# Optimization experiments

Measured on AMD Instinct MI355X. Metric: run time of the kernel, lower is better.

## Reference

```python
import jax, jax.numpy as jnp
import numpy as np

NUM_HEADS = 8
HEAD_DIM = 64  # embed_dim 512 / 8 heads


def setup_inputs() -> dict:
    key = jax.random.key(0)
    k1, k2, k3 = jax.random.split(key, 3)
    B, S, D = 2, 4096, 512
    # xavier-uniform-ish scales for faithfulness to init (values don't affect math)
    x = jax.random.normal(k1, (B, S, D), dtype=jnp.float32)
    qkv_w = jax.random.normal(k2, (3 * D, D), dtype=jnp.float32) * (1.0 / np.sqrt(D))
    qkv_b = jnp.zeros((3 * D,), dtype=jnp.float32)
    o_w = jax.random.normal(k3, (D, D), dtype=jnp.float32) * (1.0 / np.sqrt(D))
    o_b = jnp.zeros((D,), dtype=jnp.float32)
    return {"x": x, "qkv_w": qkv_w, "qkv_b": qkv_b, "o_w": o_w, "o_b": o_b}


def reference(x, qkv_w, qkv_b, o_w, o_b):
    B, S, D = x.shape
    H, hd = NUM_HEADS, HEAD_DIM
    # qkv projection: torch Linear is x @ W^T + b
    qkv = jnp.einsum('bsd,ed->bse', x, qkv_w) + qkv_b        # [B, S, 3D]
    qkv = qkv.reshape(B, S, H, 3 * hd).transpose(0, 2, 1, 3)  # [B, H, S, 3hd]
    q, k, v = jnp.split(qkv, 3, axis=-1)                      # each [B, H, S, hd]
    scale = 1.0 / jnp.sqrt(jnp.float32(hd))
    logits = jnp.einsum('bhqd,bhkd->bhqk', q, k) * scale      # [B, H, S, S]
    attn = jax.nn.softmax(logits, axis=-1)
    vals = jnp.einsum('bhqk,bhkd->bhqd', attn, v)             # [B, H, S, hd]
    vals = vals.transpose(0, 2, 1, 3).reshape(B, S, D)        # [B, S, D]
    o = jnp.einsum('bsd,ed->bse', vals, o_w) + o_b            # [B, S, D]
    return o
```

## Files before the change

kernel.cpp:

```cpp
#include <hip/hip_runtime.h>
#include <hip/hip_bf16.h>


typedef __attribute__((ext_vector_type(8)))  __bf16 bf16x8;
typedef __attribute__((ext_vector_type(2)))  __bf16 bf16x2;
typedef __attribute__((ext_vector_type(4))) float  f32x4;
typedef __attribute__((ext_vector_type(16))) float  f32x16;

__device__ __forceinline__ unsigned cvtpk(float a, float b) {
    bf16x2 t; t.x = (__bf16)a; t.y = (__bf16)b;
    union { bf16x2 v; unsigned u; } u; u.v = t; return u.u;
}
#if __has_builtin(__builtin_amdgcn_exp2f)
__device__ __forceinline__ float fexp2(float x) { return __builtin_amdgcn_exp2f(x); }
#else
__device__ __forceinline__ float fexp2(float x) { return exp2f(x); }
#endif
__device__ __forceinline__ void gload16(const unsigned short* g, unsigned short* l) {
    __builtin_amdgcn_global_load_lds(
        (const __attribute__((address_space(1))) void*)g,
        (__attribute__((address_space(3))) void*)l, 16, 0, 0);
}

__device__ __forceinline__ int swz(int row, int col) {
    return row * 64 + (col ^ ((row & 7) << 3));
}

__global__ __launch_bounds__(256) void qkv_qk_gemm(
    const float* __restrict__ X, const float* __restrict__ W,
    const float* __restrict__ bias,
    unsigned short* __restrict__ Qb, unsigned short* __restrict__ Kb)
{
    __shared__ __attribute__((aligned(16))) unsigned short SH[128 * 144];
    unsigned short* As = &SH[0];
    unsigned short* Bs = &SH[8192];
    const int tid = threadIdx.x;
    const int wid = tid >> 6, lane = tid & 63;
    const int hi = lane >> 4, lo = lane & 15;
    const int wm = wid >> 1, wn = wid & 1;
    const int m0 = blockIdx.x * 128;
    const int by3 = blockIdx.y & 3, tt = blockIdx.y >> 2;
    const float QSCL = 0.125f * 1.44269504088896f;
    const float sc = (tt == 0) ? QSCL : 1.0f;

    f32x4 acc[4][4] = {};

    for (int k0 = 0; k0 < 512; k0 += 64) {
        __syncthreads();
        #pragma unroll
        for (int i = 0; i < 8; ++i) {
            const int c = i * 256 + tid;
            const int row = c >> 4, kc = (c & 15) << 2;
            const float4 va = *(const float4*)(X + (size_t)(m0 + row) * 512 + k0 + kc);
            uint2 pa; pa.x = cvtpk(va.x, va.y); pa.y = cvtpk(va.z, va.w);
            *(uint2*)&As[swz(row, kc)] = pa;
            const int nW = (by3 * 2 + (row >> 6)) * 192 + tt * 64 + (row & 63);
            const float4 vb = *(const float4*)(W + (size_t)nW * 512 + k0 + kc);
            uint2 pb; pb.x = cvtpk(vb.x, vb.y); pb.y = cvtpk(vb.z, vb.w);
            *(uint2*)&Bs[swz(row, kc)] = pb;
        }
        __syncthreads();
        #pragma unroll
        for (int ks = 0; ks < 2; ++ks) {
            bf16x8 af[4], bfr[4];
            #pragma unroll
            for (int mi = 0; mi < 4; ++mi)
                af[mi] = *(const bf16x8*)&As[swz(wm * 64 + mi * 16 + lo, ks * 32 + hi * 8)];
            #pragma unroll
            for (int ni = 0; ni < 4; ++ni)
                bfr[ni] = *(const bf16x8*)&Bs[swz(wn * 64 + ni * 16 + lo, ks * 32 + hi * 8)];
            #pragma unroll
            for (int mi = 0; mi < 4; ++mi)
                #pragma unroll
                for (int ni = 0; ni < 4; ++ni)
                    acc[mi][ni] = __builtin_amdgcn_mfma_f32_16x16x32_bf16(
                        bfr[ni], af[mi], acc[mi][ni], 0, 0, 0);
        }
    }
    __syncthreads();

    {
        const int hq = by3 * 2 + wn;
        #pragma unroll
        for (int ni = 0; ni < 4; ++ni) {
            const float4 bv4 = *(const float4*)&bias[hq * 192 + tt * 64 + ni * 16 + hi * 4];
            #pragma unroll
            for (int mi = 0; mi < 4; ++mi) {
                const int srow_ = wm * 64 + mi * 16 + lo;
                uint2 w;
                w.x = cvtpk((acc[mi][ni][0] + bv4.x) * sc, (acc[mi][ni][1] + bv4.y) * sc);
                w.y = cvtpk((acc[mi][ni][2] + bv4.z) * sc, (acc[mi][ni][3] + bv4.w) * sc);
                *(uint2*)&SH[srow_ * 144 + wn * 72 + ni * 16 + hi * 4] = w;
            }
        }
    }
    __syncthreads();

    const int b = m0 >> 12, sb = m0 & 4095;
    unsigned short* dst = tt ? Kb : Qb;
    #pragma unroll
    for (int c = 0; c < 2; ++c) {
        const int h = by3 * 2 + c;
        #pragma unroll
        for (int qq = 0; qq < 4; ++qq) {
            const int slot = qq * 256 + tid;
            const int row = slot >> 3, g = slot & 7;
            const uint4 v = *(const uint4*)&SH[row * 144 + c * 72 + g * 8];
            *(uint4*)(dst + (((size_t)(b * 8 + h)) * 4096 + sb + row) * 64 + g * 8) = v;
        }
    }
}

__global__ __launch_bounds__(256) void qkv_v_gemm(
    const float* __restrict__ X, const float* __restrict__ W,
    const float* __restrict__ bias, unsigned short* __restrict__ Vtg)
{
    __shared__ __attribute__((aligned(16))) unsigned short SH[128 * 144];
    unsigned short* As = &SH[0];
    unsigned short* Bs = &SH[8192];
    const int tid = threadIdx.x;
    const int wid = tid >> 6, lane = tid & 63;
    const int hi = lane >> 4, lo = lane & 15;
    const int wm = wid >> 1, wn = wid & 1;
    const int m0 = blockIdx.x * 128;
    const int by = blockIdx.y;

    f32x4 acc[4][4] = {};

    for (int k0 = 0; k0 < 512; k0 += 64) {
        __syncthreads();
        #pragma unroll
        for (int i = 0; i < 8; ++i) {
            const int c = i * 256 + tid;
            const int row = c >> 4, kc = (c & 15) << 2;
            const float4 va = *(const float4*)(X + (size_t)(m0 + row) * 512 + k0 + kc);
            uint2 pa; pa.x = cvtpk(va.x, va.y); pa.y = cvtpk(va.z, va.w);
            *(uint2*)&As[swz(row, kc)] = pa;
            const int nW = (by * 2 + (row >> 6)) * 192 + 128 + (row & 63);
            const float4 vb = *(const float4*)(W + (size_t)nW * 512 + k0 + kc);
            uint2 pb; pb.x = cvtpk(vb.x, vb.y); pb.y = cvtpk(vb.z, vb.w);
            *(uint2*)&Bs[swz(row, kc)] = pb;
        }
        __syncthreads();
        #pragma unroll
        for (int ks = 0; ks < 2; ++ks) {
            bf16x8 af[4], bfr[4];
            #pragma unroll
            for (int mi = 0; mi < 4; ++mi)
                af[mi] = *(const bf16x8*)&As[swz(wm * 64 + mi * 16 + lo, ks * 32 + hi * 8)];
            #pragma unroll
            for (int ni = 0; ni < 4; ++ni)
                bfr[ni] = *(const bf16x8*)&Bs[swz(wn * 64 + ni * 16 + lo, ks * 32 + hi * 8)];
            #pragma unroll
            for (int mi = 0; mi < 4; ++mi)
                #pragma unroll
                for (int ni = 0; ni < 4; ++ni)
                    acc[mi][ni] = __builtin_amdgcn_mfma_f32_16x16x32_bf16(
                        af[mi], bfr[ni], acc[mi][ni], 0, 0, 0);
        }
    }
    __syncthreads();

    #pragma unroll
    for (int ni = 0; ni < 4; ++ni) {
        const int d = ni * 16 + lo;
        const float bv = bias[(by * 2 + wn) * 192 + 128 + d];
        #pragma unroll
        for (int mi = 0; mi < 4; ++mi) {
            const int ml = wm * 64 + mi * 16 + hi * 4;
            uint2 w;
            w.x = cvtpk(acc[mi][ni][0] + bv, acc[mi][ni][1] + bv);
            w.y = cvtpk(acc[mi][ni][2] + bv, acc[mi][ni][3] + bv);
            *(uint2*)&SH[wn * 8704 + d * 136 + ml] = w;
        }
    }
    __syncthreads();

    const int b = m0 >> 12, sb = m0 & 4095;
    #pragma unroll
    for (int qq = 0; qq < 8; ++qq) {
        const int slot = qq * 256 + tid;
        const int c = slot >> 10, d = (slot >> 4) & 63, gc = slot & 15;
        const int h = by * 2 + c;
        const uint4 v = *(const uint4*)&SH[c * 8704 + d * 136 + gc * 8];
        *(uint4*)(Vtg + ((size_t)((b * 8 + h) * 64 + d)) * 4096 + sb + gc * 8) = v;
    }
}

__global__ __launch_bounds__(512, 2) void attn_fwd(
    const unsigned short* __restrict__ Qb,
    const unsigned short* __restrict__ Kb,
    const unsigned short* __restrict__ Vtg,
    unsigned short* __restrict__ Ob)
{
    __shared__ __attribute__((aligned(16))) unsigned short smem[6][4096];

    const int tid = threadIdx.x;
    const int wid = tid >> 6, lane = tid & 63;
    const int l31 = lane & 31, hl = lane >> 5;
    const int n_ = blockIdx.x;
    const int bh = (n_ & 7) * 2 + ((n_ >> 3) & 1);
    const int qb = n_ >> 4;
    const int b = bh >> 3, h = bh & 7;
    const int q0 = qb * 256 + wid * 32;
    const size_t kbase = (size_t)bh * 4096 * 64;
    const size_t vbase = (size_t)bh * 64 * 4096;

    const int srow = tid >> 3;
    const int sg = (tid & 7) ^ (srow & 7);
    const unsigned short* kS = Kb + kbase + (size_t)srow * 64 + sg * 8;
    const unsigned short* vS = Vtg + vbase + (size_t)srow * 4096 + sg * 8;

    bf16x8 qf[4];
    #pragma unroll
    for (int dk = 0; dk < 4; ++dk)
        qf[dk] = *(const bf16x8*)(Qb + kbase + (size_t)(q0 + l31) * 64 + dk * 16 + hl * 8);

    f32x16 o0 = {}, o1 = {};
    float l_run = 0.0f;

    const int s7 = l31 & 7;
    const int baseA = l31 * 64, baseB = (32 + l31) * 64;
    const int hl4 = hl * 4;

    gload16(kS, &smem[0][tid * 8]);
    gload16(vS, &smem[3][tid * 8]);
    gload16(kS + 4096, &smem[1][tid * 8]);
    gload16(vS + 64, &smem[4][tid * 8]);
    asm volatile("s_waitcnt vmcnt(2)" ::: "memory");
    __builtin_amdgcn_s_barrier();
    __builtin_amdgcn_sched_barrier(0);

    for (int t = 0; t < 64; ++t) {
        const int cur = t % 3;
        if (t < 62) {
            const int nb = (t + 2) % 3;
            gload16(kS + (size_t)(t + 2) * 4096, &smem[nb][tid * 8]);
            gload16(vS + (size_t)(t + 2) * 64, &smem[3 + nb][tid * 8]);
        }
        const unsigned short* KT = &smem[cur][0];
        const unsigned short* VT = &smem[3 + cur][0];

        f32x16 s0 = {}, s1 = {};
        __builtin_amdgcn_s_setprio(1);
        #pragma unroll
        for (int dk = 0; dk < 4; ++dk) {
            const int g = dk * 2 + hl;
            const bf16x8 kA = *(const bf16x8*)(KT + baseA + 8 * (g ^ s7));
            const bf16x8 kB = *(const bf16x8*)(KT + baseB + 8 * (g ^ s7));
            s0 = __builtin_amdgcn_mfma_f32_32x32x16_bf16(kA, qf[dk], s0, 0, 0, 0);
            s1 = __builtin_amdgcn_mfma_f32_32x32x16_bf16(kB, qf[dk], s1, 0, 0, 0);
        }
        __builtin_amdgcn_s_setprio(0);

        #pragma unroll
        for (int i = 0; i < 16; ++i) {
            s0[i] = fexp2(s0[i]);
            s1[i] = fexp2(s1[i]);
        }
        float lsA = 0.f, lsB = 0.f, lsC = 0.f, lsD = 0.f;
        #pragma unroll
        for (int i = 0; i < 4; ++i) {
            lsA += s0[i];      lsB += s0[i + 4];
            lsA += s0[i + 8];  lsB += s0[i + 12];
            lsC += s1[i];      lsD += s1[i + 4];
            lsC += s1[i + 8];  lsD += s1[i + 12];
        }
        l_run += (lsA + lsB) + (lsC + lsD);

        union U8 { unsigned u[4]; bf16x8 v; };
        U8 p0, p1, p2, p3;
        #pragma unroll
        for (int i = 0; i < 4; ++i) {
            p0.u[i] = cvtpk(s0[2 * i],     s0[2 * i + 1]);
            p1.u[i] = cvtpk(s0[2 * i + 8], s0[2 * i + 9]);
            p2.u[i] = cvtpk(s1[2 * i],     s1[2 * i + 1]);
            p3.u[i] = cvtpk(s1[2 * i + 8], s1[2 * i + 9]);
        }
        const bf16x8 pf[4] = { p0.v, p1.v, p2.v, p3.v };

        __builtin_amdgcn_s_setprio(1);
        #pragma unroll
        for (int ks = 0; ks < 4; ++ks) {
            const int gA = ((2 * ks) ^ s7) << 3, gB = ((2 * ks + 1) ^ s7) << 3;
            union { uint2 u2[2]; bf16x8 v; } va, vb;
            va.u2[0] = *(const uint2*)(VT + baseA + gA + hl4);
            va.u2[1] = *(const uint2*)(VT + baseA + gB + hl4);
            vb.u2[0] = *(const uint2*)(VT + baseB + gA + hl4);
            vb.u2[1] = *(const uint2*)(VT + baseB + gB + hl4);
            o0 = __builtin_amdgcn_mfma_f32_32x32x16_bf16(va.v, pf[ks], o0, 0, 0, 0);
            o1 = __builtin_amdgcn_mfma_f32_32x32x16_bf16(vb.v, pf[ks], o1, 0, 0, 0);
        }
        __builtin_amdgcn_s_setprio(0);

        if (t < 63) {
            if (t < 62) asm volatile("s_waitcnt vmcnt(2)" ::: "memory");
            else        asm volatile("s_waitcnt vmcnt(0)" ::: "memory");
            __builtin_amdgcn_s_barrier();
            __builtin_amdgcn_sched_barrier(0);
        }
    }
    __builtin_amdgcn_s_barrier();
    __builtin_amdgcn_sched_barrier(0);

    l_run += __shfl_xor(l_run, 32);
    unsigned short* Ew = &smem[wid >> 1][(wid & 1) * 2048];
    const int prow = l31 * 64;
    const float inv = 1.0f / l_run;
    #pragma unroll
    for (int u = 0; u < 4; ++u) {
        uint2 w0, w1;
        w0.x = cvtpk(o0[4 * u] * inv, o0[4 * u + 1] * inv);
        w0.y = cvtpk(o0[4 * u + 2] * inv, o0[4 * u + 3] * inv);
        *(uint2*)&Ew[prow + ((u ^ s7) << 3) + (hl << 2)] = w0;
        w1.x = cvtpk(o1[4 * u] * inv, o1[4 * u + 1] * inv);
        w1.y = cvtpk(o1[4 * u + 2] * inv, o1[4 * u + 3] * inv);
        *(uint2*)&Ew[prow + (((4 + u) ^ s7) << 3) + (hl << 2)] = w1;
    }
    asm volatile("s_waitcnt lgkmcnt(0)" ::: "memory");
    __builtin_amdgcn_sched_barrier(0);
    #pragma unroll
    for (int rr = 0; rr < 4; ++rr) {
        const int qrow = (lane >> 3) + rr * 8;
        const int gphys = (lane & 7) ^ (qrow & 7);
        const uint4 v = *(const uint4*)&Ew[qrow * 64 + gphys * 8];
        *(uint4*)(Ob + ((size_t)b * 4096 + q0 + qrow) * 512 + h * 64 + (lane & 7) * 8) = v;
    }
}

__global__ __launch_bounds__(256) void oproj_gemm(
    const unsigned short* __restrict__ A, const float* __restrict__ W,
    const float* __restrict__ bias, float* __restrict__ C)
{
    __shared__ __attribute__((aligned(16))) unsigned short As[128 * 64];
    __shared__ __attribute__((aligned(16))) unsigned short Bs[128 * 64];
    const int tid = threadIdx.x;
    const int wid = tid >> 6, lane = tid & 63;
    const int hi = lane >> 4, lo = lane & 15;
    const int wm = wid >> 1, wn = wid & 1;
    const int m0 = blockIdx.x * 128, n0 = blockIdx.y * 128;

    f32x4 acc[4][4] = {};
    for (int k0 = 0; k0 < 512; k0 += 64) {
        __syncthreads();
        #pragma unroll
        for (int i = 0; i < 4; ++i) {
            const int c = i * 256 + tid;
            const int row = c >> 3, kc = (c & 7) << 3;
            *(uint4*)&As[swz(row, kc)] =
                *(const uint4*)(A + (size_t)(m0 + row) * 512 + k0 + kc);
        }
        #pragma unroll
        for (int i = 0; i < 8; ++i) {
            const int c = i * 256 + tid;
            const int row = c >> 4, kc = (c & 15) << 2;
            const float4 vb = *(const float4*)(W + (size_t)(n0 + row) * 512 + k0 + kc);
            uint2 pb; pb.x = cvtpk(vb.x, vb.y); pb.y = cvtpk(vb.z, vb.w);
            *(uint2*)&Bs[swz(row, kc)] = pb;
        }
        __syncthreads();
        #pragma unroll
        for (int ks = 0; ks < 2; ++ks) {
            bf16x8 af[4], bfr[4];
            #pragma unroll
            for (int mi = 0; mi < 4; ++mi)
                af[mi] = *(const bf16x8*)&As[swz(wm * 64 + mi * 16 + lo, ks * 32 + hi * 8)];
            #pragma unroll
            for (int ni = 0; ni < 4; ++ni)
                bfr[ni] = *(const bf16x8*)&Bs[swz(wn * 64 + ni * 16 + lo, ks * 32 + hi * 8)];
            #pragma unroll
            for (int mi = 0; mi < 4; ++mi)
                #pragma unroll
                for (int ni = 0; ni < 4; ++ni)
                    acc[mi][ni] = __builtin_amdgcn_mfma_f32_16x16x32_bf16(
                        af[mi], bfr[ni], acc[mi][ni], 0, 0, 0);
        }
    }

    #pragma unroll
    for (int mi = 0; mi < 4; ++mi) {
        #pragma unroll
        for (int ni = 0; ni < 4; ++ni) {
            const int n = n0 + wn * 64 + ni * 16 + lo;
            const float bv = bias[n];
            #pragma unroll
            for (int j = 0; j < 4; ++j) {
                const int m = m0 + wm * 64 + mi * 16 + hi * 4 + j;
                C[(size_t)m * 512 + n] = acc[mi][ni][j] + bv;
            }
        }
    }
}

extern "C" void kernel_launch(void* const* d_in, const int* in_sizes, int n_in,
                              void* d_out, int out_size, void* d_ws, size_t ws_size,
                              hipStream_t stream) {
    const float* x     = (const float*)d_in[0];
    const float* qkv_w = (const float*)d_in[1];
    const float* qkv_b = (const float*)d_in[2];
    const float* o_w   = (const float*)d_in[3];
    const float* o_b   = (const float*)d_in[4];
    float* out = (float*)d_out;

    const size_t NELEM = (size_t)2 * 8 * 4096 * 64;
    unsigned short* Qb  = (unsigned short*)d_ws;
    unsigned short* Kb  = Qb + NELEM;
    unsigned short* Vtg = Kb + NELEM;
    unsigned short* Ob  = Vtg + NELEM;

    qkv_qk_gemm<<<dim3(64, 8), 256, 0, stream>>>(x, qkv_w, qkv_b, Qb, Kb);
    qkv_v_gemm<<<dim3(64, 4), 256, 0, stream>>>(x, qkv_w, qkv_b, Vtg);
    attn_fwd<<<dim3(256), 512, 0, stream>>>(Qb, Kb, Vtg, Ob);
    oproj_gemm<<<dim3(64, 4), 256, 0, stream>>>(Ob, o_w, o_b, out);
}
```

Baseline: 131.4 us.

## Double-buffer four KV tiles per barrier and permute V columns for single 16-byte reads

The attention loop now loads groups of four K/V tiles into one half of a double buffer and synchronises once per group instead of once per tile. The old design was a three-stage ring with a wait and barrier after every tile. The V-transpose writer is changed to store columns permuted so that each lane's PV operand is one contiguous 16-byte LDS read instead of two 8-byte reads. Shared memory grows from 48KB to 128KB, which limits blocks per CU and may break the two-blocks launch bound. The loads for the next group are waited on fully at each group end, so prefetch depth is one group.

Result: faster. 124.2 us (-5.5%).

```diff
diff --git a/kernel.cpp b/kernel.cpp
--- a/kernel.cpp
+++ b/kernel.cpp
@@ -80,9 +80,9 @@
     __syncthreads();
 
     {
-        const int hq = by3 * 2 + wn;
         #pragma unroll
         for (int ni = 0; ni < 4; ++ni) {
+            const int hq = by3 * 2 + wn;
             const float4 bv4 = *(const float4*)&bias[hq * 192 + tt * 64 + ni * 16 + hi * 4];
             #pragma unroll
             for (int mi = 0; mi < 4; ++mi) {
@@ -180,10 +180,13 @@
     #pragma unroll
     for (int qq = 0; qq < 8; ++qq) {
         const int slot = qq * 256 + tid;
-        const int c = slot >> 10, d = (slot >> 4) & 63, gc = slot & 15;
+        const int c = slot >> 10, d = (slot >> 4) & 63, mb = slot & 15;
+        const int src = c * 8704 + d * 136 + 16 * (mb >> 1) + 4 * (mb & 1);
+        const uint2 a  = *(const uint2*)&SH[src];
+        const uint2 bb = *(const uint2*)&SH[src + 8];
+        uint4 w; w.x = a.x; w.y = a.y; w.z = bb.x; w.w = bb.y;
         const int h = by * 2 + c;
-        const uint4 v = *(const uint4*)&SH[c * 8704 + d * 136 + gc * 8];
-        *(uint4*)(Vtg + ((size_t)((b * 8 + h) * 64 + d)) * 4096 + sb + gc * 8) = v;
+        *(uint4*)(Vtg + ((size_t)((b * 8 + h) * 64 + d)) * 4096 + sb + 8 * mb) = w;
     }
 }
 
@@ -193,7 +196,7 @@
     const unsigned short* __restrict__ Vtg,
     unsigned short* __restrict__ Ob)
 {
-    __shared__ __attribute__((aligned(16))) unsigned short smem[6][4096];
+    __shared__ __attribute__((aligned(16))) unsigned short smem[2][4][2][4096];
 
     const int tid = threadIdx.x;
     const int wid = tid >> 6, lane = tid & 63;
@@ -221,90 +224,88 @@
 
     const int s7 = l31 & 7;
     const int baseA = l31 * 64, baseB = (32 + l31) * 64;
-    const int hl4 = hl * 4;
-
-    gload16(kS, &smem[0][tid * 8]);
-    gload16(vS, &smem[3][tid * 8]);
-    gload16(kS + 4096, &smem[1][tid * 8]);
-    gload16(vS + 64, &smem[4][tid * 8]);
-    asm volatile("s_waitcnt vmcnt(2)" ::: "memory");
+    const int ldst = tid * 8;
+
+    #pragma unroll
+    for (int i = 0; i < 4; ++i) {
+        gload16(kS + (size_t)i * 4096, &smem[0][i][0][ldst]);
+        gload16(vS + (size_t)i * 64,   &smem[0][i][1][ldst]);
+    }
+    asm volatile("s_waitcnt vmcnt(0)" ::: "memory");
     __builtin_amdgcn_s_barrier();
     __builtin_amdgcn_sched_barrier(0);
 
-    for (int t = 0; t < 64; ++t) {
-        const int cur = t % 3;
-        if (t < 62) {
-            const int nb = (t + 2) % 3;
-            gload16(kS + (size_t)(t + 2) * 4096, &smem[nb][tid * 8]);
-            gload16(vS + (size_t)(t + 2) * 64, &smem[3 + nb][tid * 8]);
-        }
-        const unsigned short* KT = &smem[cur][0];
-        const unsigned short* VT = &smem[3 + cur][0];
-
-        f32x16 s0 = {}, s1 = {};
-        __builtin_amdgcn_s_setprio(1);
-        #pragma unroll
-        for (int dk = 0; dk < 4; ++dk) {
-            const int g = dk * 2 + hl;
-            const bf16x8 kA = *(const bf16x8*)(KT + baseA + 8 * (g ^ s7));
-            const bf16x8 kB = *(const bf16x8*)(KT + baseB + 8 * (g ^ s7));
-            s0 = __builtin_amdgcn_mfma_f32_32x32x16_bf16(kA, qf[dk], s0, 0, 0, 0);
-            s1 = __builtin_amdgcn_mfma_f32_32x32x16_bf16(kB, qf[dk], s1, 0, 0, 0);
-        }
-        __builtin_amdgcn_s_setprio(0);
-
-        #pragma unroll
-        for (int i = 0; i < 16; ++i) {
-            s0[i] = fexp2(s0[i]);
-            s1[i] = fexp2(s1[i]);
-        }
-        float lsA = 0.f, lsB = 0.f, lsC = 0.f, lsD = 0.f;
-        #pragma unroll
-        for (int i = 0; i < 4; ++i) {
-            lsA += s0[i];      lsB += s0[i + 4];
-            lsA += s0[i + 8];  lsB += s0[i + 12];
-            lsC += s1[i];      lsD += s1[i + 4];
-            lsC += s1[i + 8];  lsD += s1[i + 12];
-        }
-        l_run += (lsA + lsB) + (lsC + lsD);
-
-        union U8 { unsigned u[4]; bf16x8 v; };
-        U8 p0, p1, p2, p3;
-        #pragma unroll
-        for (int i = 0; i < 4; ++i) {
-            p0.u[i] = cvtpk(s0[2 * i],     s0[2 * i + 1]);
-            p1.u[i] = cvtpk(s0[2 * i + 8], s0[2 * i + 9]);
-            p2.u[i] = cvtpk(s1[2 * i],     s1[2 * i + 1]);
-            p3.u[i] = cvtpk(s1[2 * i + 8], s1[2 * i + 9]);
-        }
-        const bf16x8 pf[4] = { p0.v, p1.v, p2.v, p3.v };
-
-        __builtin_amdgcn_s_setprio(1);
-        #pragma unroll
-        for (int ks = 0; ks < 4; ++ks) {
-            const int gA = ((2 * ks) ^ s7) << 3, gB = ((2 * ks + 1) ^ s7) << 3;
-            union { uint2 u2[2]; bf16x8 v; } va, vb;
-            va.u2[0] = *(const uint2*)(VT + baseA + gA + hl4);
-            va.u2[1] = *(const uint2*)(VT + baseA + gB + hl4);
-            vb.u2[0] = *(const uint2*)(VT + baseB + gA + hl4);
-            vb.u2[1] = *(const uint2*)(VT + baseB + gB + hl4);
-            o0 = __builtin_amdgcn_mfma_f32_32x32x16_bf16(va.v, pf[ks], o0, 0, 0, 0);
-            o1 = __builtin_amdgcn_mfma_f32_32x32x16_bf16(vb.v, pf[ks], o1, 0, 0, 0);
-        }
-        __builtin_amdgcn_s_setprio(0);
-
-        if (t < 63) {
-            if (t < 62) asm volatile("s_waitcnt vmcnt(2)" ::: "memory");
-            else        asm volatile("s_waitcnt vmcnt(0)" ::: "memory");
-            __builtin_amdgcn_s_barrier();
-            __builtin_amdgcn_sched_barrier(0);
-        }
-    }
-    __builtin_amdgcn_s_barrier();
-    __builtin_amdgcn_sched_barrier(0);
+    for (int g = 0; g < 16; ++g) {
+        const int cur = g & 1;
+        if (g < 15) {
+            #pragma unroll
+            for (int i = 0; i < 4; ++i) {
+                const size_t T = 4 * (g + 1) + i;
+                gload16(kS + T * 4096, &smem[cur ^ 1][i][0][ldst]);
+                gload16(vS + T * 64,   &smem[cur ^ 1][i][1][ldst]);
+            }
+        }
+        #pragma unroll
+        for (int ti = 0; ti < 4; ++ti) {
+            const unsigned short* KT = &smem[cur][ti][0][0];
+            const unsigned short* VT = &smem[cur][ti][1][0];
+
+            f32x16 s0 = {}, s1 = {};
+            __builtin_amdgcn_s_setprio(1);
+            #pragma unroll
+            for (int dk = 0; dk < 4; ++dk) {
+                const int gk = dk * 2 + hl;
+                const bf16x8 kA = *(const bf16x8*)(KT + baseA + 8 * (gk ^ s7));
+                const bf16x8 kB = *(const bf16x8*)(KT + baseB + 8 * (gk ^ s7));
+                s0 = __builtin_amdgcn_mfma_f32_32x32x16_bf16(kA, qf[dk], s0, 0, 0, 0);
+                s1 = __builtin_amdgcn_mfma_f32_32x32x16_bf16(kB, qf[dk], s1, 0, 0, 0);
+            }
+            __builtin_amdgcn_s_setprio(0);
+
+            #pragma unroll
+            for (int i = 0; i < 16; ++i) {
+                s0[i] = fexp2(s0[i]);
+                s1[i] = fexp2(s1[i]);
+            }
+            float lsA = 0.f, lsB = 0.f, lsC = 0.f, lsD = 0.f;
+            #pragma unroll
+            for (int i = 0; i < 4; ++i) {
+                lsA += s0[i];      lsB += s0[i + 4];
+                lsA += s0[i + 8];  lsB += s0[i + 12];
+                lsC += s1[i];      lsD += s1[i + 4];
+                lsC += s1[i + 8];  lsD += s1[i + 12];
+            }
+            l_run += (lsA + lsB) + (lsC + lsD);
+
+            union U8 { unsigned u[4]; bf16x8 v; };
+            U8 p0, p1, p2, p3;
+            #pragma unroll
+            for (int i = 0; i < 4; ++i) {
+                p0.u[i] = cvtpk(s0[2 * i],     s0[2 * i + 1]);
+                p1.u[i] = cvtpk(s0[2 * i + 8], s0[2 * i + 9]);
+                p2.u[i] = cvtpk(s1[2 * i],     s1[2 * i + 1]);
+                p3.u[i] = cvtpk(s1[2 * i + 8], s1[2 * i + 9]);
+            }
+            const bf16x8 pf[4] = { p0.v, p1.v, p2.v, p3.v };
+
+            __builtin_amdgcn_s_setprio(1);
+            #pragma unroll
+            for (int ks = 0; ks < 4; ++ks) {
+                const int gv = ((2 * ks + hl) ^ s7) << 3;
+                const bf16x8 va = *(const bf16x8*)(VT + baseA + gv);
+                const bf16x8 vb = *(const bf16x8*)(VT + baseB + gv);
+                o0 = __builtin_amdgcn_mfma_f32_32x32x16_bf16(va, pf[ks], o0, 0, 0, 0);
+                o1 = __builtin_amdgcn_mfma_f32_32x32x16_bf16(vb, pf[ks], o1, 0, 0, 0);
+            }
+            __builtin_amdgcn_s_setprio(0);
+        }
+        asm volatile("s_waitcnt vmcnt(0)" ::: "memory");
+        __builtin_amdgcn_s_barrier();
+        __builtin_amdgcn_sched_barrier(0);
+    }
 
     l_run += __shfl_xor(l_run, 32);
-    unsigned short* Ew = &smem[wid >> 1][(wid & 1) * 2048];
+    unsigned short* Ew = &smem[0][0][0][0] + wid * 2048;
     const int prow = l31 * 64;
     const float inv = 1.0f / l_run;
     #pragma unroll
```
